# Optimization experiments

Hardware: AMD Instinct MI355X
Metric: run time of the kernel (lower is better)

## Reference

```python
import jax, jax.numpy as jnp
import numpy as np

HEADS = 8
DIM_HEAD = 64
SCALE = DIM_HEAD ** -0.5


def setup_inputs() -> dict:
    key = jax.random.key(0)
    k1, k2, k3 = jax.random.split(key, 3)
    b, n, dim = 2, 4096, 512
    inner = HEADS * DIM_HEAD
    x = jax.random.normal(k1, (b, n, dim), dtype=jnp.float32)
    w_qkv = jax.random.normal(k2, (dim, 3 * inner), dtype=jnp.float32) * (dim ** -0.5)
    w_out = jax.random.normal(k3, (inner, dim), dtype=jnp.float32) * (inner ** -0.5)
    b_out = jnp.zeros((dim,), dtype=jnp.float32)
    return {"x": x, "w_qkv": w_qkv, "w_out": w_out, "b_out": b_out}


def reference(x, w_qkv, w_out, b_out):
    b, n, dim = x.shape
    qkv = x @ w_qkv  # [b, n, 3*inner]
    q, k, v = jnp.split(qkv, 3, axis=-1)
    # b n (h d) -> b h n d
    split_heads = lambda t: t.reshape(b, n, HEADS, DIM_HEAD).transpose(0, 2, 1, 3)
    q, k, v = split_heads(q), split_heads(k), split_heads(v)
    dots = jnp.einsum('bhid,bhjd->bhij', q, k) * SCALE  # [b, h, n, n]
    attn = jax.nn.log_softmax(dots, axis=-1)  # NOTE: log-softmax, not softmax
    out = jnp.einsum('bhij,bhjd->bhid', attn, v)  # [b, h, n, d]
    out = out.transpose(0, 2, 1, 3).reshape(b, n, HEADS * DIM_HEAD)
    return out @ w_out + b_out + x
```

## Files before the change

### kernel.cpp

```cpp
#include <hip/hip_runtime.h>
#include <stdint.h>

#define NSEQ   4096
#define BATCH  2
#define NHEAD  8
#define DHEAD  64
#define DIM    512
#define NQKV   1536
#define MROWS  (BATCH*NSEQ)
#define NBH    (BATCH*NHEAD)

typedef float  f32x4 __attribute__((ext_vector_type(4)));
typedef short  s16x8 __attribute__((ext_vector_type(8)));

__device__ __forceinline__ unsigned short f2b(float f){
  unsigned int u = __float_as_uint(f);
  u += 0x7FFFu + ((u >> 16) & 1u);
  return (unsigned short)(u >> 16);
}
__device__ __forceinline__ float b2f(unsigned short h){
  return __uint_as_float(((unsigned int)h) << 16);
}
__device__ __forceinline__ void gld_lds16(const void* g, void* l){
  __builtin_amdgcn_global_load_lds((const __attribute__((address_space(1))) unsigned int*)g,
                                   (__attribute__((address_space(3))) unsigned int*)l, 16, 0, 0);
}
__device__ __forceinline__ float fexp2(float x){
  return __uint_as_float((unsigned)(int)__builtin_fmaf(x, 8388608.f, 1064866805.f));
}

__global__ void k_prep(const float* __restrict__ x, unsigned short* __restrict__ xb,
                       const float* __restrict__ wqkv, unsigned short* __restrict__ wqT,
                       const float* __restrict__ wout, unsigned short* __restrict__ woT){
  __shared__ float t[32][33];
  const int b = blockIdx.x;
  if (b < 4096){
    const int i = b*256 + threadIdx.x;
    float4 v = ((const float4*)x)[i];
    ushort4 o;
    o.x = f2b(v.x); o.y = f2b(v.y); o.z = f2b(v.z); o.w = f2b(v.w);
    ((ushort4*)xb)[i] = o;
  } else {
    const float* in; unsigned short* out; int R, C, cb, rb;
    if (b < 4096 + 768){
      const int q = b - 4096; in = wqkv; out = wqT; R = DIM; C = NQKV;
      cb = (q % 48)*32; rb = (q / 48)*32;
    } else {
      const int q = b - 4096 - 768; in = wout; out = woT; R = DIM; C = DIM;
      cb = (q & 15)*32; rb = (q >> 4)*32;
    }
    const int tx = threadIdx.x & 31, ty = threadIdx.x >> 5;
    #pragma unroll
    for (int s = 0; s < 32; s += 8) t[ty+s][tx] = in[(size_t)(rb+ty+s)*C + cb + tx];
    __syncthreads();
    #pragma unroll
    for (int s = 0; s < 32; s += 8) out[(size_t)(cb+ty+s)*R + rb + tx] = f2b(t[tx][ty+s]);
  }
}

#define QSTAGE(KS, B) do{ \
    const int k0_ = (KS)*32; \
    _Pragma("unroll") \
    for (int i_ = 0; i_ < 2; ++i_){ \
      const int slot_ = w*2 + i_; \
      const int r_ = slot_*16 + (lane>>2); \
      const int ch_ = (lane&3) ^ (r_&3); \
      gld_lds16(A  + (size_t)(m0+r_)*DIM + k0_ + ch_*8, (char*)at[B] + slot_*1024); \
      gld_lds16(Bt + (size_t)(n0+r_)*DIM + k0_ + ch_*8, (char*)bt[B] + slot_*1024); \
    }}while(0)

__global__ __launch_bounds__(256) void k_qkv_gemm(
    const unsigned short* __restrict__ A,
    const unsigned short* __restrict__ Bt,
    unsigned short* __restrict__ qbuf, unsigned short* __restrict__ kbuf,
    unsigned short* __restrict__ vbuf){
  __shared__ __align__(16) unsigned short at[2][128*32];
  __shared__ __align__(16) unsigned short bt[2][128*32];
  const int n0 = blockIdx.x*128, m0 = blockIdx.y*128;
  const int tid = threadIdx.x, w = tid>>6, lane = tid&63;
  const int wr = (w>>1)*64, wc = (w&1)*64;
  f32x4 acc[4][4] = {};
  QSTAGE(0, 0);
  for (int ks = 0; ks < 16; ++ks){
    __syncthreads();
    if (ks < 15) QSTAGE(ks+1, (ks+1)&1);
    const unsigned short* atc = at[ks&1];
    const unsigned short* btc = bt[ks&1];
    s16x8 af[4], bfr[4];
    #pragma unroll
    for (int f = 0; f < 4; ++f){
      const int rr = wr + f*16 + (lane&15);
      af[f]  = *(const s16x8*)((const char*)atc + rr*64 + ((((lane>>4)) ^ (rr&3))<<4));
      const int cc = wc + f*16 + (lane&15);
      bfr[f] = *(const s16x8*)((const char*)btc + cc*64 + ((((lane>>4)) ^ (cc&3))<<4));
    }
    #pragma unroll
    for (int fr = 0; fr < 4; ++fr)
      #pragma unroll
      for (int fc = 0; fc < 4; ++fc)
        acc[fr][fc] = __builtin_amdgcn_mfma_f32_16x16x32_bf16(bfr[fc], af[fr], acc[fr][fc], 0,0,0);
  }
  const float QS = 0.18033688011112042f;
  #pragma unroll
  for (int fr = 0; fr < 4; ++fr){
    const int row = m0 + wr + fr*16 + (lane&15);
    const int b = row >> 12, n = row & 4095;
    #pragma unroll
    for (int fc = 0; fc < 4; ++fc){
      const int col0 = n0 + wc + fc*16 + ((lane>>4)<<2);
      const int which = col0 >> 9;
      const int h = (col0 & 511) >> 6;
      const int d = col0 & 63;
      unsigned short* dst = (which==0) ? qbuf : ((which==1) ? kbuf : vbuf);
      const float sc = (which==0) ? QS : 1.f;
      ushort4 o;
      o.x = f2b(acc[fr][fc][0]*sc);
      o.y = f2b(acc[fr][fc][1]*sc);
      o.z = f2b(acc[fr][fc][2]*sc);
      o.w = f2b(acc[fr][fc][3]*sc);
      *(ushort4*)(dst + (size_t)((b*NHEAD + h)*NSEQ + n)*DHEAD + d) = o;
    }
  }
}

__global__ __launch_bounds__(256) void k_tpart(
    const unsigned short* __restrict__ kbuf, const unsigned short* __restrict__ vbuf,
    float* __restrict__ tpartf, float* __restrict__ vsp){
  __shared__ __align__(16) unsigned short kt[64*64];
  __shared__ __align__(16) unsigned short vt[64*64];
  const int bh = blockIdx.y, jc = blockIdx.x;
  const unsigned short* K = kbuf + (size_t)bh*NSEQ*DHEAD;
  const unsigned short* V = vbuf + (size_t)bh*NSEQ*DHEAD;
  const int tid = threadIdx.x;
  const int d1 = (tid>>4)<<2, d2 = (tid&15)<<2;
  float accT[4][4] = {{0.f}};
  float accV[4] = {0.f,0.f,0.f,0.f};
  for (int st = 0; st < 4; ++st){
    const int j0 = jc*256 + st*64;
    __syncthreads();
    #pragma unroll
    for (int c = 0; c < 2; ++c){
      const int q = tid + 256*c;
      const int row = q>>3, ch = q&7;
      *(float4*)((char*)kt + row*128 + ch*16) = *(const float4*)((const char*)K + (size_t)(j0+row)*128 + ch*16);
      *(float4*)((char*)vt + row*128 + ch*16) = *(const float4*)((const char*)V + (size_t)(j0+row)*128 + ch*16);
    }
    __syncthreads();
    for (int jj = 0; jj < 64; ++jj){
      const ushort4 k4 = *(const ushort4*)(kt + jj*64 + d1);
      const ushort4 v4 = *(const ushort4*)(vt + jj*64 + d2);
      float kf[4] = {b2f(k4.x), b2f(k4.y), b2f(k4.z), b2f(k4.w)};
      float vf[4] = {b2f(v4.x), b2f(v4.y), b2f(v4.z), b2f(v4.w)};
      #pragma unroll
      for (int a = 0; a < 4; ++a)
        #pragma unroll
        for (int b = 0; b < 4; ++b) accT[a][b] += kf[a]*vf[b];
      #pragma unroll
      for (int b = 0; b < 4; ++b) accV[b] += vf[b];
    }
  }
  float* tp = tpartf + ((size_t)bh*16 + jc)*4096;
  #pragma unroll
  for (int a = 0; a < 4; ++a){
    float4 o; o.x = accT[a][0]; o.y = accT[a][1]; o.z = accT[a][2]; o.w = accT[a][3];
    *(float4*)&tp[(d1+a)*64 + d2] = o;
  }
  if (tid < 16){
    #pragma unroll
    for (int b = 0; b < 4; ++b) vsp[((size_t)bh*16 + jc)*64 + d2 + b] = accV[b];
  }
}

__global__ void k_tred(const float* __restrict__ tpartf, const float* __restrict__ vsp,
                       unsigned short* __restrict__ TB, float* __restrict__ vsum){
  const int blk = blockIdx.x;
  const int bh = blk >> 4, part = blk & 15;
  const int tid = threadIdx.x;
  const int idx = part*256 + tid;
  const int dd1 = idx>>6, dd2 = idx&63;
  float s = 0.f;
  #pragma unroll
  for (int pr = 0; pr < 16; ++pr) s += tpartf[((size_t)bh*16 + pr)*4096 + idx];
  TB[(size_t)bh*4096 + dd2*64 + dd1] = f2b(s);
  if (part == 0 && tid < 64){
    float v = 0.f;
    #pragma unroll
    for (int pr = 0; pr < 16; ++pr) v += vsp[((size_t)bh*16 + pr)*64 + tid];
    vsum[bh*64 + tid] = v;
  }
}

#define ASTAGE(U, BUFI) do { \
    const int ti_ = jbase + (((U)+phase)&15); \
    const size_t o_ = (size_t)ti_*64*DHEAD; \
    char* d_ = (char*)kt[BUFI]; \
    gld_lds16(kg0 + o_, d_ + s0*1024); \
    gld_lds16(kg1 + o_, d_ + s1*1024); } while(0)

#define ATILE(BUFI) do { \
    const char* buf_ = (const char*)kt[BUFI]; \
    _Pragma("unroll") \
    for (int kk = 0; kk < 4; ++kk){ \
      const int r_ = kk*16 + (lane&15); \
      const s16x8 b0_ = *(const s16x8*)(buf_ + r_*128 + ((((lane>>4))   ^ (r_&7))<<4)); \
      const s16x8 b1_ = *(const s16x8*)(buf_ + r_*128 + (((4+(lane>>4)) ^ (r_&7))<<4)); \
      f32x4 a0_ = {0.f,0.f,0.f,0.f}, a1_ = {0.f,0.f,0.f,0.f}; \
      f32x4 a2_ = {0.f,0.f,0.f,0.f}, a3_ = {0.f,0.f,0.f,0.f}; \
      __builtin_amdgcn_s_setprio(1); \
      a0_ = __builtin_amdgcn_mfma_f32_16x16x32_bf16(aq[0][0], b0_, a0_, 0,0,0); \
      a0_ = __builtin_amdgcn_mfma_f32_16x16x32_bf16(aq[0][1], b1_, a0_, 0,0,0); \
      a1_ = __builtin_amdgcn_mfma_f32_16x16x32_bf16(aq[1][0], b0_, a1_, 0,0,0); \
      a1_ = __builtin_amdgcn_mfma_f32_16x16x32_bf16(aq[1][1], b1_, a1_, 0,0,0); \
      a2_ = __builtin_amdgcn_mfma_f32_16x16x32_bf16(aq[2][0], b0_, a2_, 0,0,0); \
      a2_ = __builtin_amdgcn_mfma_f32_16x16x32_bf16(aq[2][1], b1_, a2_, 0,0,0); \
      a3_ = __builtin_amdgcn_mfma_f32_16x16x32_bf16(aq[3][0], b0_, a3_, 0,0,0); \
      a3_ = __builtin_amdgcn_mfma_f32_16x16x32_bf16(aq[3][1], b1_, a3_, 0,0,0); \
      __builtin_amdgcn_s_setprio(0); \
      _Pragma("unroll") \
      for (int rr = 0; rr < 4; ++rr){ \
        lsum[0][rr] += __builtin_amdgcn_exp2f(a0_[rr]); \
        lsum[1][rr] += __builtin_amdgcn_exp2f(a1_[rr]); \
        lsum[2][rr] += __builtin_amdgcn_exp2f(a2_[rr]); \
        lsum[3][rr] += fexp2(a3_[rr]); \
      } \
    } } while(0)

#define APHASE(U) do { \
    if ((U) <= 13)      { asm volatile("s_waitcnt vmcnt(4)" ::: "memory"); } \
    else if ((U) == 14) { asm volatile("s_waitcnt vmcnt(2)" ::: "memory"); } \
    else                { asm volatile("s_waitcnt vmcnt(0)" ::: "memory"); } \
    __builtin_amdgcn_s_barrier(); \
    asm volatile("" ::: "memory"); \
    if ((U) <= 12) ASTAGE((U)+3, ((U)+3)&3); \
    ATILE((U)&3); } while(0)

__global__ __launch_bounds__(256) void k_attn(
    const unsigned short* __restrict__ qbuf, const unsigned short* __restrict__ kbuf,
    float* __restrict__ ps){
  __shared__ __align__(16) unsigned short kt[4][64*64];
  const int bid = blockIdx.x;
  const int idx = bid >> 3;
  const int bh  = ((bid & 7) << 1) + (idx >> 6);
  const int rest = idx & 63;
  const int qchunk = rest >> 2;
  const int js = rest & 3;
  const int tid = threadIdx.x, w = tid>>6, lane = tid&63;
  const int q0 = qchunk*256 + w*64;
  const unsigned short* Q = qbuf + (size_t)bh*NSEQ*DHEAD;
  const unsigned short* K = kbuf + (size_t)bh*NSEQ*DHEAD;

  s16x8 aq[4][2];
  #pragma unroll
  for (int g = 0; g < 4; ++g){
    const int qrow = q0 + g*16 + (lane&15);
    aq[g][0] = *(const s16x8*)(Q + (size_t)qrow*DHEAD + ((lane>>4)<<3));
    aq[g][1] = *(const s16x8*)(Q + (size_t)qrow*DHEAD + 32 + ((lane>>4)<<3));
  }

  const int s0 = w*2, s1 = w*2 + 1;
  const int srow0 = s0*8 + (lane>>3), srow1 = s1*8 + (lane>>3);
  const int sch = ((lane&7) ^ (lane>>3));
  const unsigned short* kg0 = K + (size_t)srow0*DHEAD + sch*8;
  const unsigned short* kg1 = K + (size_t)srow1*DHEAD + sch*8;

  const int phase = (idx*5) & 15;
  const int jbase = js*16;

  ASTAGE(0, 0);
  ASTAGE(1, 1);
  ASTAGE(2, 2);

  float lsum[4][4] = {};
  APHASE(0);  APHASE(1);  APHASE(2);  APHASE(3);
  APHASE(4);  APHASE(5);  APHASE(6);  APHASE(7);
  APHASE(8);  APHASE(9);  APHASE(10); APHASE(11);
  APHASE(12); APHASE(13); APHASE(14); APHASE(15);

  #pragma unroll
  for (int m = 1; m < 16; m <<= 1)
    #pragma unroll
    for (int g = 0; g < 4; ++g)
      #pragma unroll
      for (int r = 0; r < 4; ++r) lsum[g][r] += __shfl_xor(lsum[g][r], m, 16);

  if ((lane&15) == 0){
    float* pp = ps + ((size_t)js*NBH + bh)*NSEQ;
    #pragma unroll
    for (int g = 0; g < 4; ++g)
      #pragma unroll
      for (int r = 0; r < 4; ++r)
        pp[q0 + g*16 + (lane>>4)*4 + r] = lsum[g][r];
  }
}

__global__ __launch_bounds__(256) void k_attn_fin(
    const unsigned short* __restrict__ qbuf, const unsigned short* __restrict__ TB,
    const float* __restrict__ vsum, const float* __restrict__ ps,
    unsigned short* __restrict__ om){
  const int bid = blockIdx.x;
  const int bh = bid >> 6, qchunk = bid & 63;
  const int tid = threadIdx.x, w = tid>>6, lane = tid&63;
  const int q0 = qchunk*64 + w*16;
  const unsigned short* Q = qbuf + (size_t)bh*NSEQ*DHEAD;
  const int qrow = q0 + (lane&15);
  const s16x8 aq0 = *(const s16x8*)(Q + (size_t)qrow*DHEAD + ((lane>>4)<<3));
  const s16x8 aq1 = *(const s16x8*)(Q + (size_t)qrow*DHEAD + 32 + ((lane>>4)<<3));
  const float* p0 = ps + (size_t)bh*NSEQ;
  const float* p1 = ps + ((size_t)NBH   + bh)*NSEQ;
  const float* p2 = ps + ((size_t)2*NBH + bh)*NSEQ;
  const float* p3 = ps + ((size_t)3*NBH + bh)*NSEQ;
  float lse2[4];
  #pragma unroll
  for (int r = 0; r < 4; ++r){
    const int n = q0 + (lane>>4)*4 + r;
    lse2[r] = log2f((p0[n] + p1[n]) + (p2[n] + p3[n]));
  }
  const unsigned short* tb = TB + (size_t)bh*4096;
  const int b = bh>>3, h = bh&7;
  #pragma unroll
  for (int fc = 0; fc < 4; ++fc){
    const int d2 = fc*16 + (lane&15);
    const s16x8 t0 = *(const s16x8*)(tb + d2*64 + ((lane>>4)<<3));
    const s16x8 t1 = *(const s16x8*)(tb + d2*64 + 32 + ((lane>>4)<<3));
    const float vs = vsum[bh*64 + d2];
    f32x4 acc = {0.f,0.f,0.f,0.f};
    acc = __builtin_amdgcn_mfma_f32_16x16x32_bf16(aq0, t0, acc, 0,0,0);
    acc = __builtin_amdgcn_mfma_f32_16x16x32_bf16(aq1, t1, acc, 0,0,0);
    #pragma unroll
    for (int r = 0; r < 4; ++r){
      const int n = q0 + (lane>>4)*4 + r;
      const float val = 0.6931471805599453f * (acc[r] - lse2[r]*vs);
      om[((size_t)b*NSEQ + n)*DIM + h*DHEAD + d2] = f2b(val);
    }
  }
}

#define OSTAGE(KS, B) do{ \
    const int k0_ = (KS)*32; \
    _Pragma("unroll") \
    for (int i_ = 0; i_ < 2; ++i_){ \
      const int slot_ = w*2 + i_; \
      const int r_ = slot_*16 + (lane>>2); \
      const int ch_ = (lane&3) ^ (r_&3); \
      gld_lds16(A  + (size_t)(m0+r_)*DIM + k0_ + ch_*8, (char*)at[B] + slot_*1024); \
      gld_lds16(Bt + (size_t)(n0+r_)*DIM + k0_ + ch_*8, (char*)bt[B] + slot_*1024); \
    }}while(0)

__global__ __launch_bounds__(256) void k_out_gemm(
    const unsigned short* __restrict__ A,
    const unsigned short* __restrict__ Bt,
    const float* __restrict__ bias, const float* __restrict__ xres,
    float* __restrict__ out){
  __shared__ __align__(16) unsigned short at[2][128*32];
  __shared__ __align__(16) unsigned short bt[2][128*32];
  const int n0 = blockIdx.x*128, m0 = blockIdx.y*128;
  const int tid = threadIdx.x, w = tid>>6, lane = tid&63;
  const int wr = (w>>1)*64, wc = (w&1)*64;
  f32x4 acc[4][4] = {};
  OSTAGE(0, 0);
  for (int ks = 0; ks < 16; ++ks){
    __syncthreads();
    if (ks < 15) OSTAGE(ks+1, (ks+1)&1);
    const unsigned short* atc = at[ks&1];
    const unsigned short* btc = bt[ks&1];
    s16x8 af[4], bfr[4];
    #pragma unroll
    for (int f = 0; f < 4; ++f){
      const int rr = wr + f*16 + (lane&15);
      af[f]  = *(const s16x8*)((const char*)atc + rr*64 + ((((lane>>4)) ^ (rr&3))<<4));
      const int cc = wc + f*16 + (lane&15);
      bfr[f] = *(const s16x8*)((const char*)btc + cc*64 + ((((lane>>4)) ^ (cc&3))<<4));
    }
    #pragma unroll
    for (int fr = 0; fr < 4; ++fr)
      #pragma unroll
      for (int fc = 0; fc < 4; ++fc)
        acc[fr][fc] = __builtin_amdgcn_mfma_f32_16x16x32_bf16(bfr[fc], af[fr], acc[fr][fc], 0,0,0);
  }
  #pragma unroll
  for (int fr = 0; fr < 4; ++fr){
    const int row = m0 + wr + fr*16 + (lane&15);
    #pragma unroll
    for (int fc = 0; fc < 4; ++fc){
      const int col0 = n0 + wc + fc*16 + ((lane>>4)<<2);
      const float4 bb = *(const float4*)&bias[col0];
      const float4 xr = *(const float4*)&xres[(size_t)row*DIM + col0];
      float4 o;
      o.x = acc[fr][fc][0] + bb.x + xr.x;
      o.y = acc[fr][fc][1] + bb.y + xr.y;
      o.z = acc[fr][fc][2] + bb.z + xr.z;
      o.w = acc[fr][fc][3] + bb.w + xr.w;
      *(float4*)&out[(size_t)row*DIM + col0] = o;
    }
  }
}

extern "C" void kernel_launch(void* const* d_in, const int* in_sizes, int n_in,
                              void* d_out, int out_size, void* d_ws, size_t ws_size,
                              hipStream_t stream){
  const float* x    = (const float*)d_in[0];
  const float* wqkv = (const float*)d_in[1];
  const float* wout = (const float*)d_in[2];
  const float* bout = (const float*)d_in[3];
  float* out = (float*)d_out;

  char* p = (char*)d_ws;
  unsigned short* xb   = (unsigned short*)p; p += (size_t)MROWS*DIM*2;
  unsigned short* wqT  = (unsigned short*)p; p += (size_t)NQKV*DIM*2;
  unsigned short* woT  = (unsigned short*)p; p += (size_t)DIM*DIM*2;
  unsigned short* qbuf = (unsigned short*)p; p += (size_t)NBH*NSEQ*DHEAD*2;
  unsigned short* kbuf = (unsigned short*)p; p += (size_t)NBH*NSEQ*DHEAD*2;
  unsigned short* vbuf = (unsigned short*)p; p += (size_t)NBH*NSEQ*DHEAD*2;
  float* tpartf        = (float*)p;          p += (size_t)NBH*16*4096*4;
  float* vsp           = (float*)p;          p += (size_t)NBH*16*64*4;
  unsigned short* TB   = (unsigned short*)p; p += (size_t)NBH*64*64*2;
  float* vsum          = (float*)p;          p += (size_t)NBH*64*4;
  unsigned short* om   = (unsigned short*)p; p += (size_t)MROWS*DIM*2;
  float* ps            = (float*)p;          p += (size_t)4*NBH*NSEQ*4;

  k_prep<<<dim3(4096 + 768 + 256), dim3(256), 0, stream>>>(x, xb, wqkv, wqT, wout, woT);
  k_qkv_gemm<<<dim3(NQKV/128, MROWS/128), dim3(256), 0, stream>>>(xb, wqT, qbuf, kbuf, vbuf);
  k_tpart<<<dim3(16, NBH), dim3(256), 0, stream>>>(kbuf, vbuf, tpartf, vsp);
  k_tred<<<dim3(256), dim3(256), 0, stream>>>(tpartf, vsp, TB, vsum);
  k_attn<<<dim3(1024), dim3(256), 0, stream>>>(qbuf, kbuf, ps);
  k_attn_fin<<<dim3(1024), dim3(256), 0, stream>>>(qbuf, TB, vsum, ps, om);
  k_out_gemm<<<dim3(DIM/128, MROWS/128), dim3(256), 0, stream>>>(om, woT, bout, x, out);
}
```

Measured before the change: 122.9 us.

## Fuse attention finalization into k_attn via last-block atomic counter

Result: slower. 217.0 us (+76.5%).

```diff
diff --git a/kernel.cpp b/kernel.cpp
--- a/kernel.cpp
+++ b/kernel.cpp
@@ -172,10 +172,12 @@
 }
 
 __global__ void k_tred(const float* __restrict__ tpartf, const float* __restrict__ vsp,
-                       unsigned short* __restrict__ TB, float* __restrict__ vsum){
+                       unsigned short* __restrict__ TB, float* __restrict__ vsum,
+                       int* __restrict__ done){
   const int blk = blockIdx.x;
   const int bh = blk >> 4, part = blk & 15;
   const int tid = threadIdx.x;
+  if (tid == 0) done[blk] = 0;
   const int idx = part*256 + tid;
   const int dd1 = idx>>6, dd2 = idx&63;
   float s = 0.f;
@@ -236,8 +238,11 @@
 
 __global__ __launch_bounds__(256) void k_attn(
     const unsigned short* __restrict__ qbuf, const unsigned short* __restrict__ kbuf,
-    float* __restrict__ ps){
+    const unsigned short* __restrict__ TB, const float* __restrict__ vsum,
+    float* __restrict__ ps, int* __restrict__ done,
+    unsigned short* __restrict__ om){
   __shared__ __align__(16) unsigned short kt[4][64*64];
+  __shared__ int lastflag;
   const int bid = blockIdx.x;
   const int idx = bid >> 3;
   const int bh  = ((bid & 7) << 1) + (idx >> 6);
@@ -291,30 +296,25 @@
       for (int r = 0; r < 4; ++r)
         pp[q0 + g*16 + (lane>>4)*4 + r] = lsum[g][r];
   }
-}
-
-__global__ __launch_bounds__(256) void k_attn_fin(
-    const unsigned short* __restrict__ qbuf, const unsigned short* __restrict__ TB,
-    const float* __restrict__ vsum, const float* __restrict__ ps,
-    unsigned short* __restrict__ om){
-  const int bid = blockIdx.x;
-  const int bh = bid >> 6, qchunk = bid & 63;
-  const int tid = threadIdx.x, w = tid>>6, lane = tid&63;
-  const int q0 = qchunk*64 + w*16;
-  const unsigned short* Q = qbuf + (size_t)bh*NSEQ*DHEAD;
-  const int qrow = q0 + (lane&15);
-  const s16x8 aq0 = *(const s16x8*)(Q + (size_t)qrow*DHEAD + ((lane>>4)<<3));
-  const s16x8 aq1 = *(const s16x8*)(Q + (size_t)qrow*DHEAD + 32 + ((lane>>4)<<3));
+
+  __threadfence();
+  if (tid == 0) lastflag = atomicAdd(&done[bh*16 + qchunk], 1);
+  __syncthreads();
+  if (lastflag != 3) return;
+  __threadfence();
+
   const float* p0 = ps + (size_t)bh*NSEQ;
   const float* p1 = ps + ((size_t)NBH   + bh)*NSEQ;
   const float* p2 = ps + ((size_t)2*NBH + bh)*NSEQ;
   const float* p3 = ps + ((size_t)3*NBH + bh)*NSEQ;
-  float lse2[4];
-  #pragma unroll
-  for (int r = 0; r < 4; ++r){
-    const int n = q0 + (lane>>4)*4 + r;
-    lse2[r] = log2f((p0[n] + p1[n]) + (p2[n] + p3[n]));
-  }
+  float lse2[4][4];
+  #pragma unroll
+  for (int g = 0; g < 4; ++g)
+    #pragma unroll
+    for (int r = 0; r < 4; ++r){
+      const int n = q0 + g*16 + (lane>>4)*4 + r;
+      lse2[g][r] = log2f((p0[n] + p1[n]) + (p2[n] + p3[n]));
+    }
   const unsigned short* tb = TB + (size_t)bh*4096;
   const int b = bh>>3, h = bh&7;
   #pragma unroll
@@ -323,14 +323,17 @@
     const s16x8 t0 = *(const s16x8*)(tb + d2*64 + ((lane>>4)<<3));
     const s16x8 t1 = *(const s16x8*)(tb + d2*64 + 32 + ((lane>>4)<<3));
     const float vs = vsum[bh*64 + d2];
-    f32x4 acc = {0.f,0.f,0.f,0.f};
-    acc = __builtin_amdgcn_mfma_f32_16x16x32_bf16(aq0, t0, acc, 0,0,0);
-    acc = __builtin_amdgcn_mfma_f32_16x16x32_bf16(aq1, t1, acc, 0,0,0);
-    #pragma unroll
-    for (int r = 0; r < 4; ++r){
-      const int n = q0 + (lane>>4)*4 + r;
-      const float val = 0.6931471805599453f * (acc[r] - lse2[r]*vs);
-      om[((size_t)b*NSEQ + n)*DIM + h*DHEAD + d2] = f2b(val);
+    #pragma unroll
+    for (int g = 0; g < 4; ++g){
+      f32x4 acc = {0.f,0.f,0.f,0.f};
+      acc = __builtin_amdgcn_mfma_f32_16x16x32_bf16(aq[g][0], t0, acc, 0,0,0);
+      acc = __builtin_amdgcn_mfma_f32_16x16x32_bf16(aq[g][1], t1, acc, 0,0,0);
+      #pragma unroll
+      for (int r = 0; r < 4; ++r){
+        const int n = q0 + g*16 + (lane>>4)*4 + r;
+        const float val = 0.6931471805599453f * (acc[r] - lse2[g][r]*vs);
+        om[((size_t)b*NSEQ + n)*DIM + h*DHEAD + d2] = f2b(val);
+      }
     }
   }
 }
@@ -417,12 +420,12 @@
   float* vsum          = (float*)p;          p += (size_t)NBH*64*4;
   unsigned short* om   = (unsigned short*)p; p += (size_t)MROWS*DIM*2;
   float* ps            = (float*)p;          p += (size_t)4*NBH*NSEQ*4;
+  int* done            = (int*)p;            p += 256*4;
 
   k_prep<<<dim3(4096 + 768 + 256), dim3(256), 0, stream>>>(x, xb, wqkv, wqT, wout, woT);
   k_qkv_gemm<<<dim3(NQKV/128, MROWS/128), dim3(256), 0, stream>>>(xb, wqT, qbuf, kbuf, vbuf);
   k_tpart<<<dim3(16, NBH), dim3(256), 0, stream>>>(kbuf, vbuf, tpartf, vsp);
-  k_tred<<<dim3(256), dim3(256), 0, stream>>>(tpartf, vsp, TB, vsum);
-  k_attn<<<dim3(1024), dim3(256), 0, stream>>>(qbuf, kbuf, ps);
-  k_attn_fin<<<dim3(1024), dim3(256), 0, stream>>>(qbuf, TB, vsum, ps, om);
+  k_tred<<<dim3(256), dim3(256), 0, stream>>>(tpartf, vsp, TB, vsum, done);
+  k_attn<<<dim3(1024), dim3(256), 0, stream>>>(qbuf, kbuf, TB, vsum, ps, done, om);
   k_out_gemm<<<dim3(DIM/128, MROWS/128), dim3(256), 0, stream>>>(om, woT, bout, x, out);
 }
```
